# Performance work log

Hardware: AMD Instinct MI355X
Metric: run time of the kernel (lower is better)

Reference implementation:

```python
import jax, jax.numpy as jnp
import numpy as np

N = 2_097_152   # total pixels (e.g., 8 images of 512x512)
C = 32          # feature channels
NUM_SEG = 8192  # number of superpixels (max label + 1)


def setup_inputs() -> dict:
    key = jax.random.key(0)
    k1, k2 = jax.random.split(key)
    x = jax.random.normal(k1, (N, C), dtype=jnp.float32)
    sp = jax.random.randint(k2, (N,), 0, NUM_SEG, dtype=jnp.int64)
    return {"input": x, "superpixels": sp, "num_segments": NUM_SEG}


def reference(input, superpixels, num_segments):
    # Segment mean: scatter-add features and counts by superpixel label, then divide.
    sums = jax.ops.segment_sum(input, superpixels, num_segments=num_segments)  # [S, C]
    counts = jax.ops.segment_sum(
        jnp.ones((input.shape[0],), dtype=input.dtype), superpixels,
        num_segments=num_segments)  # [S]
    # Guard empty segments (original would produce 0/0; we define mean of empty as 0).
    average = sums / jnp.maximum(counts, 1.0)[:, None]
    return average
```

## Files before the change

kernel.cpp:

```cpp
#include <hip/hip_runtime.h>


constexpr int C = 32;
constexpr int CAP = 1024;

typedef float v4f __attribute__((ext_vector_type(4)));

__global__ void scatter_bucket_kernel(const int4* __restrict__ sp4,
                                      int* __restrict__ cursor,
                                      int* __restrict__ order,
                                      int n4) {
    int t = blockIdx.x * blockDim.x + threadIdx.x;
    if (t >= n4) return;
    int4 v = sp4[t];
    int p = t << 2;
    int p0 = atomicAdd(&cursor[v.x], 1);
    int p1 = atomicAdd(&cursor[v.y], 1);
    int p2 = atomicAdd(&cursor[v.z], 1);
    int p3 = atomicAdd(&cursor[v.w], 1);
    if (p0 < CAP) order[v.x * CAP + p0] = p;
    if (p1 < CAP) order[v.y * CAP + p1] = p + 1;
    if (p2 < CAP) order[v.z * CAP + p2] = p + 2;
    if (p3 < CAP) order[v.w * CAP + p3] = p + 3;
}

__global__ __launch_bounds__(256) void segment_mean_kernel(const v4f* __restrict__ x4,
                                                           const int* __restrict__ order,
                                                           const int* __restrict__ cursor,
                                                           v4f* __restrict__ out4, int S) {
    const int wave = threadIdx.x >> 6;
    const int wt   = threadIdx.x & 63;
    const int s    = blockIdx.x * 4 + wave;
    if (s >= S) return;
    const int cnt   = cursor[s];
    const int lim   = (cnt < CAP) ? cnt : CAP;
    const int start = s * CAP;
    const int slot  = wt >> 3;
    const int cg    = wt & 7;

    v4f acc = {0.f, 0.f, 0.f, 0.f};
    int i = slot;
    for (; i + 24 < lim; i += 32) {
        int p0 = order[start + i];
        int p1 = order[start + i + 8];
        int p2 = order[start + i + 16];
        int p3 = order[start + i + 24];
        v4f v0 = __builtin_nontemporal_load(&x4[p0 * 8 + cg]);
        v4f v1 = __builtin_nontemporal_load(&x4[p1 * 8 + cg]);
        v4f v2 = __builtin_nontemporal_load(&x4[p2 * 8 + cg]);
        v4f v3 = __builtin_nontemporal_load(&x4[p3 * 8 + cg]);
        acc += v0 + v1 + v2 + v3;
    }
    for (; i < lim; i += 8) {
        int p = order[start + i];
        acc += __builtin_nontemporal_load(&x4[p * 8 + cg]);
    }
    #pragma unroll
    for (int d = 32; d >= 8; d >>= 1) {
        acc.x += __shfl_down(acc.x, d);
        acc.y += __shfl_down(acc.y, d);
        acc.z += __shfl_down(acc.z, d);
        acc.w += __shfl_down(acc.w, d);
    }
    if (wt < 8) {
        float inv = (cnt > 0) ? 1.0f / (float)cnt : 0.0f;
        out4[s * 8 + wt] = acc * inv;
    }
}

__global__ void fb_scatter_kernel(const float* __restrict__ x, const int* __restrict__ sp,
                                  float* __restrict__ sums, float* __restrict__ fcounts,
                                  int n_pixels) {
    long long t = (long long)blockIdx.x * blockDim.x + threadIdx.x;
    long long p = t >> 5;
    int c = (int)(t & 31);
    if (p >= n_pixels) return;
    int label = sp[p];
    float v = x[p * C + c];
    atomicAdd(&sums[(long long)label * C + c], v);
    if (c == 0) atomicAdd(&fcounts[label], 1.0f);
}
__global__ void fb_divide_kernel(float* __restrict__ out, const float* __restrict__ fcounts,
                                 int total) {
    int t = blockIdx.x * blockDim.x + threadIdx.x;
    if (t >= total) return;
    out[t] = out[t] / fmaxf(fcounts[t >> 5], 1.0f);
}

extern "C" void kernel_launch(void* const* d_in, const int* in_sizes, int n_in,
                              void* d_out, int out_size, void* d_ws, size_t ws_size,
                              hipStream_t stream) {
    const float* x  = (const float*)d_in[0];
    const int*   sp = (const int*)d_in[1];
    const int n = in_sizes[1];
    const int S = out_size / C;

    const size_t need = (size_t)S * sizeof(int) + (size_t)S * CAP * sizeof(int);
    if (ws_size >= need && (n & 3) == 0) {
        int* cursor = (int*)d_ws;
        int* order  = cursor + S;

        hipMemsetAsync(cursor, 0, (size_t)S * sizeof(int), stream);
        const int n4 = n >> 2;
        scatter_bucket_kernel<<<(n4 + 255) / 256, 256, 0, stream>>>(
            (const int4*)sp, cursor, order, n4);
        segment_mean_kernel<<<(S + 3) / 4, 256, 0, stream>>>(
            (const v4f*)x, order, cursor, (v4f*)d_out, S);
    } else {
        float* sums    = (float*)d_out;
        float* fcounts = (float*)d_ws;
        hipMemsetAsync(d_out, 0, sizeof(float) * (size_t)out_size, stream);
        hipMemsetAsync(fcounts, 0, sizeof(float) * (size_t)S, stream);
        long long total_threads = (long long)n * C;
        fb_scatter_kernel<<<dim3((unsigned)((total_threads + 255) / 256)), 256, 0, stream>>>(
            x, sp, sums, fcounts, n);
        fb_divide_kernel<<<(out_size + 255) / 256, 256, 0, stream>>>(sums, fcounts, out_size);
    }
}
```

Before: 421.3 us.

## Scatter feature rows into per-segment fp16 buckets instead of index lists

```diff
diff --git a/kernel.cpp b/kernel.cpp
--- a/kernel.cpp
+++ b/kernel.cpp
@@ -4,56 +4,69 @@
 constexpr int C = 32;
 constexpr int CAP = 1024;
 
-typedef float v4f __attribute__((ext_vector_type(4)));
+typedef float    v4f __attribute__((ext_vector_type(4)));
+typedef _Float16 h4  __attribute__((ext_vector_type(4)));
 
-__global__ void scatter_bucket_kernel(const int4* __restrict__ sp4,
-                                      int* __restrict__ cursor,
-                                      int* __restrict__ order,
-                                      int n4) {
-    int t = blockIdx.x * blockDim.x + threadIdx.x;
-    if (t >= n4) return;
-    int4 v = sp4[t];
-    int p = t << 2;
-    int p0 = atomicAdd(&cursor[v.x], 1);
-    int p1 = atomicAdd(&cursor[v.y], 1);
-    int p2 = atomicAdd(&cursor[v.z], 1);
-    int p3 = atomicAdd(&cursor[v.w], 1);
-    if (p0 < CAP) order[v.x * CAP + p0] = p;
-    if (p1 < CAP) order[v.y * CAP + p1] = p + 1;
-    if (p2 < CAP) order[v.z * CAP + p2] = p + 2;
-    if (p3 < CAP) order[v.w * CAP + p3] = p + 3;
+__global__ __launch_bounds__(256) void scatter_rows_kernel(
+    const v4f* __restrict__ x4, const int* __restrict__ sp,
+    int* __restrict__ cursor,
+    h4* __restrict__ xb,
+    int n)
+{
+    const int wave = threadIdx.x >> 6;
+    const int wt   = threadIdx.x & 63;
+    const int base = blockIdx.x * 256 + wave * 64;
+    if (base >= n) return;
+
+    const int slot = wt >> 3;
+    const int cg   = wt & 7;
+
+    const int p     = base + wt;
+    const int label = (p < n) ? sp[p] : -1;
+    int pos = 0;
+    if (label >= 0) pos = atomicAdd(&cursor[label], 1);
+
+    #pragma unroll
+    for (int k = 0; k < 8; ++k) {
+        const int src = slot * 8 + k;
+        const int lab = __shfl(label, src);
+        const int pp  = __shfl(pos, src);
+        if (lab < 0 || pp >= CAP) continue;
+        const int q = base + src;
+        v4f v = __builtin_nontemporal_load(&x4[q * 8 + cg]);
+        h4 hv = __builtin_convertvector(v, h4);
+        __builtin_nontemporal_store(hv, &xb[((size_t)lab * CAP + pp) * 8 + cg]);
+    }
 }
 
-__global__ __launch_bounds__(256) void segment_mean_kernel(const v4f* __restrict__ x4,
-                                                           const int* __restrict__ order,
-                                                           const int* __restrict__ cursor,
-                                                           v4f* __restrict__ out4, int S) {
+__global__ __launch_bounds__(256) void bucket_mean_kernel(
+    const h4* __restrict__ xb, const int* __restrict__ cursor,
+    v4f* __restrict__ out4, int S)
+{
     const int wave = threadIdx.x >> 6;
     const int wt   = threadIdx.x & 63;
     const int s    = blockIdx.x * 4 + wave;
     if (s >= S) return;
-    const int cnt   = cursor[s];
-    const int lim   = (cnt < CAP) ? cnt : CAP;
-    const int start = s * CAP;
-    const int slot  = wt >> 3;
-    const int cg    = wt & 7;
+
+    const int cnt = cursor[s];
+    const int lim = (cnt < CAP) ? cnt : CAP;
+    const h4* row = xb + (size_t)s * CAP * 8;
+    const int slot = wt >> 3;
+    const int cg   = wt & 7;
 
     v4f acc = {0.f, 0.f, 0.f, 0.f};
     int i = slot;
     for (; i + 24 < lim; i += 32) {
-        int p0 = order[start + i];
-        int p1 = order[start + i + 8];
-        int p2 = order[start + i + 16];
-        int p3 = order[start + i + 24];
-        v4f v0 = __builtin_nontemporal_load(&x4[p0 * 8 + cg]);
-        v4f v1 = __builtin_nontemporal_load(&x4[p1 * 8 + cg]);
-        v4f v2 = __builtin_nontemporal_load(&x4[p2 * 8 + cg]);
-        v4f v3 = __builtin_nontemporal_load(&x4[p3 * 8 + cg]);
-        acc += v0 + v1 + v2 + v3;
+        h4 a = __builtin_nontemporal_load(&row[(size_t)(i      ) * 8 + cg]);
+        h4 b = __builtin_nontemporal_load(&row[(size_t)(i +  8) * 8 + cg]);
+        h4 c = __builtin_nontemporal_load(&row[(size_t)(i + 16) * 8 + cg]);
+        h4 d = __builtin_nontemporal_load(&row[(size_t)(i + 24) * 8 + cg]);
+        acc += __builtin_convertvector(a, v4f) + __builtin_convertvector(b, v4f)
+             + __builtin_convertvector(c, v4f) + __builtin_convertvector(d, v4f);
     }
     for (; i < lim; i += 8) {
-        int p = order[start + i];
-        acc += __builtin_nontemporal_load(&x4[p * 8 + cg]);
+        h4 a = __builtin_nontemporal_load(&row[(size_t)i * 8 + cg]);
+        acc += __builtin_convertvector(a, v4f);
     }
     #pragma unroll
     for (int d = 32; d >= 8; d >>= 1) {
@@ -95,17 +108,17 @@
     const int n = in_sizes[1];
     const int S = out_size / C;
 
-    const size_t need = (size_t)S * sizeof(int) + (size_t)S * CAP * sizeof(int);
-    if (ws_size >= need && (n & 3) == 0) {
+    const size_t need = (size_t)S * sizeof(int)
+                      + (size_t)S * CAP * C * sizeof(_Float16);
+    if (ws_size >= need) {
         int* cursor = (int*)d_ws;
-        int* order  = cursor + S;
+        h4*  xb     = (h4*)((char*)d_ws + (size_t)S * sizeof(int));
 
         hipMemsetAsync(cursor, 0, (size_t)S * sizeof(int), stream);
-        const int n4 = n >> 2;
-        scatter_bucket_kernel<<<(n4 + 255) / 256, 256, 0, stream>>>(
-            (const int4*)sp, cursor, order, n4);
-        segment_mean_kernel<<<(S + 3) / 4, 256, 0, stream>>>(
-            (const v4f*)x, order, cursor, (v4f*)d_out, S);
+        scatter_rows_kernel<<<(n + 255) / 256, 256, 0, stream>>>(
+            (const v4f*)x, sp, cursor, xb, n);
+        bucket_mean_kernel<<<(S + 3) / 4, 256, 0, stream>>>(
+            xb, cursor, (v4f*)d_out, S);
     } else {
         float* sums    = (float*)d_out;
         float* fcounts = (float*)d_ws;
```

New measurement: 452.2 us. 1.07x slower.

## Prefetch features into cache during bucketing and flip nontemporal hints

Applied to the files above, without the earlier changes.

```diff
diff --git a/kernel.cpp b/kernel.cpp
--- a/kernel.cpp
+++ b/kernel.cpp
@@ -6,22 +6,35 @@
 
 typedef float v4f __attribute__((ext_vector_type(4)));
 
-__global__ void scatter_bucket_kernel(const int4* __restrict__ sp4,
-                                      int* __restrict__ cursor,
-                                      int* __restrict__ order,
-                                      int n4) {
-    int t = blockIdx.x * blockDim.x + threadIdx.x;
-    if (t >= n4) return;
-    int4 v = sp4[t];
-    int p = t << 2;
-    int p0 = atomicAdd(&cursor[v.x], 1);
-    int p1 = atomicAdd(&cursor[v.y], 1);
-    int p2 = atomicAdd(&cursor[v.z], 1);
-    int p3 = atomicAdd(&cursor[v.w], 1);
-    if (p0 < CAP) order[v.x * CAP + p0] = p;
-    if (p1 < CAP) order[v.y * CAP + p1] = p + 1;
-    if (p2 < CAP) order[v.z * CAP + p2] = p + 2;
-    if (p3 < CAP) order[v.w * CAP + p3] = p + 3;
+__global__ __launch_bounds__(256) void scatter_bucket_kernel(
+    const int4* __restrict__ sp4, const v4f* __restrict__ x4,
+    int* __restrict__ cursor,
+    int* __restrict__ order,
+    int n4)
+{
+    const int t = blockIdx.x * blockDim.x + threadIdx.x;
+    if (t < n4) {
+        int4 v = sp4[t];
+        int p = t << 2;
+        int p0 = atomicAdd(&cursor[v.x], 1);
+        int p1 = atomicAdd(&cursor[v.y], 1);
+        int p2 = atomicAdd(&cursor[v.z], 1);
+        int p3 = atomicAdd(&cursor[v.w], 1);
+        if (p0 < CAP) __builtin_nontemporal_store(p,     &order[v.x * CAP + p0]);
+        if (p1 < CAP) __builtin_nontemporal_store(p + 1, &order[v.y * CAP + p1]);
+        if (p2 < CAP) __builtin_nontemporal_store(p + 2, &order[v.z * CAP + p2]);
+        if (p3 < CAP) __builtin_nontemporal_store(p + 3, &order[v.w * CAP + p3]);
+    }
+
+    const long long total4 = (long long)n4 * 32;
+    const long long base   = (long long)blockIdx.x * 8192 + threadIdx.x;
+    v4f acc = {0.f, 0.f, 0.f, 0.f};
+    #pragma unroll 4
+    for (int j = 0; j < 32; ++j) {
+        long long idx = base + (long long)j * 256;
+        if (idx < total4) acc += x4[idx];
+    }
+    asm volatile("" :: "v"(acc.x), "v"(acc.y), "v"(acc.z), "v"(acc.w));
 }
 
 __global__ __launch_bounds__(256) void segment_mean_kernel(const v4f* __restrict__ x4,
@@ -41,19 +54,19 @@
     v4f acc = {0.f, 0.f, 0.f, 0.f};
     int i = slot;
     for (; i + 24 < lim; i += 32) {
-        int p0 = order[start + i];
-        int p1 = order[start + i + 8];
-        int p2 = order[start + i + 16];
-        int p3 = order[start + i + 24];
-        v4f v0 = __builtin_nontemporal_load(&x4[p0 * 8 + cg]);
-        v4f v1 = __builtin_nontemporal_load(&x4[p1 * 8 + cg]);
-        v4f v2 = __builtin_nontemporal_load(&x4[p2 * 8 + cg]);
-        v4f v3 = __builtin_nontemporal_load(&x4[p3 * 8 + cg]);
+        int p0 = __builtin_nontemporal_load(&order[start + i]);
+        int p1 = __builtin_nontemporal_load(&order[start + i + 8]);
+        int p2 = __builtin_nontemporal_load(&order[start + i + 16]);
+        int p3 = __builtin_nontemporal_load(&order[start + i + 24]);
+        v4f v0 = x4[p0 * 8 + cg];
+        v4f v1 = x4[p1 * 8 + cg];
+        v4f v2 = x4[p2 * 8 + cg];
+        v4f v3 = x4[p3 * 8 + cg];
         acc += v0 + v1 + v2 + v3;
     }
     for (; i < lim; i += 8) {
-        int p = order[start + i];
-        acc += __builtin_nontemporal_load(&x4[p * 8 + cg]);
+        int p = __builtin_nontemporal_load(&order[start + i]);
+        acc += x4[p * 8 + cg];
     }
     #pragma unroll
     for (int d = 32; d >= 8; d >>= 1) {
@@ -103,7 +116,7 @@
         hipMemsetAsync(cursor, 0, (size_t)S * sizeof(int), stream);
         const int n4 = n >> 2;
         scatter_bucket_kernel<<<(n4 + 255) / 256, 256, 0, stream>>>(
-            (const int4*)sp, cursor, order, n4);
+            (const int4*)sp, (const v4f*)x, cursor, order, n4);
         segment_mean_kernel<<<(S + 3) / 4, 256, 0, stream>>>(
             (const v4f*)x, order, cursor, (v4f*)d_out, S);
     } else {
```

Result: slower. 541.1 us (+28.4%).
